# Performance work log

Hardware: AMD Instinct MI355X
Metric: run time of the kernel (lower is better)

The kernel has to match this reference:

```python
import jax, jax.numpy as jnp
import numpy as np

B, C, H, W = 16, 64, 128, 128
K = 3   # kernel_size
R = 4   # region_number
DN = ("NCHW", "OIHW", "NCHW")
PAD = [(1, 1), (1, 1)]


def leaky(x):
    return jax.nn.leaky_relu(x, 0.1)


@jax.custom_vjp
def asign_index(kernel, guide):
    # kernel: (B, R, C, H, W), guide: (B, R, H, W)
    mask = jax.nn.one_hot(jnp.argmax(guide, axis=1), guide.shape[1], axis=1, dtype=kernel.dtype)
    return jnp.sum(kernel * mask[:, :, None], axis=1)


def _asign_fwd(kernel, guide):
    return asign_index(kernel, guide), (kernel, guide)


def _asign_bwd(res, g):
    kernel, guide = res
    mask = jax.nn.one_hot(jnp.argmax(guide, axis=1), guide.shape[1], axis=1, dtype=kernel.dtype)
    grad_kernel = g[:, None] * mask[:, :, None]
    grad_guide = jnp.sum(g[:, None] * kernel, axis=2)          # (B,R,H,W)
    sm = jax.nn.softmax(guide, axis=1)                          # straight-through softmax grad
    grad_guide = sm * (grad_guide - jnp.sum(sm * grad_guide, axis=1, keepdims=True))
    return grad_kernel, grad_guide


asign_index.defvjp(_asign_fwd, _asign_bwd)


def setup_inputs() -> dict:
    key = jax.random.key(0)
    ks = jax.random.split(key, 12)
    s = 0.05
    return {
        "x0": jax.random.normal(ks[0], (B, C, H, W), jnp.float32),
        "x_deg": jax.random.normal(ks[1], (B, C), jnp.float32),
        "kw1": jax.random.normal(ks[2], (R * R, C), jnp.float32) * s,
        "kw2": jax.random.normal(ks[3], (R, C * K * K, R), jnp.float32) * s,
        "conv_w": jax.random.normal(ks[4], (C, C), jnp.float32) * s,
        "conv_b": jax.random.normal(ks[5], (C,), jnp.float32) * s,
        "ca_w1": jax.random.normal(ks[6], (R * R, C), jnp.float32) * s,
        "ca_w2": jax.random.normal(ks[7], (R, C, R), jnp.float32) * s,
        "g1_w": jax.random.normal(ks[8], (R, C, K, K), jnp.float32) * s,
        "g1_b": jax.random.normal(ks[9], (R,), jnp.float32) * s,
        "g2_w": jax.random.normal(ks[10], (R, C, K, K), jnp.float32) * s,
        "g2_b": jax.random.normal(ks[11], (R,), jnp.float32) * s,
    }


def reference(x0, x_deg, kw1, kw2, conv_w, conv_b, ca_w1, ca_w2, g1_w, g1_b, g2_w, g2_b):
    b, c, h, w = x0.shape
    # --- hypernetwork: degradation vector -> per-sample depthwise kernels ---
    h1 = leaky(x_deg @ kw1.T)                                   # (B, R*R)
    kern = jnp.einsum("bgi,goi->bgo", h1.reshape(b, R, R), kw2)  # grouped 1x1 conv1d: (B,R,C*K*K)
    kern = kern.reshape(b, R, c, K, K)
    kern = jnp.transpose(kern, (0, 2, 1, 3, 4)).reshape(b * c * R, 1, K, K)
    # per-sample-per-channel conv, R outputs per channel (groups = b*c)
    out = jax.lax.conv_general_dilated(
        x0.reshape(1, b * c, h, w), kern, (1, 1), PAD,
        dimension_numbers=DN, feature_group_count=b * c)        # (1, b*c*R, H, W)
    out = leaky(out).reshape(b, c, R, h, w).transpose(0, 2, 1, 3, 4)  # (B,R,C,H,W)
    # region routing via argmax of guide features
    guide1 = jax.lax.conv_general_dilated(x0, g1_w, (1, 1), PAD,
                                          dimension_numbers=DN) + g1_b[None, :, None, None]
    out = asign_index(out, guide1)                              # (B,C,H,W)
    # 1x1 conv (common.default_conv)
    out = jnp.einsum("bchw,oc->bohw", out, conv_w) + conv_b[None, :, None, None]
    # --- CA branch ---
    a1 = leaky(x_deg @ ca_w1.T)                                 # (B, R*R)
    att = jax.nn.sigmoid(jnp.einsum("bgi,goi->bgo", a1.reshape(b, R, R), ca_w2))  # (B,R,C)
    out2 = x0[:, None] * att[:, :, :, None, None]               # (B,R,C,H,W)
    guide2 = jax.lax.conv_general_dilated(x0, g2_w, (1, 1), PAD,
                                          dimension_numbers=DN) + g2_b[None, :, None, None]
    out2 = asign_index(out2, guide2)                            # (B,C,H,W)
    return out + out2
```

## Files before the change

kernel.cpp:

```cpp
#include <hip/hip_runtime.h>
#include <math.h>

#define Bx 16
#define Cx 64
#define Hx 128
#define Wx 128
#define HWx (Hx * Wx)

#define TW 32
#define TH 8
#define CCH 8
#define HALO_W (TW + 2)
#define HALO_H (TH + 2)
#define CPLANE (HALO_H * HALO_W)
#define CHUNK_ELEMS (CCH * CPLANE)
#define NCHUNK (Cx / CCH)

#define WS_CWB   0
#define WS_GPACK 2048
#define WS_KERN  8192
#define WS_ATT   45056

typedef short bf16x8 __attribute__((ext_vector_type(8)));
typedef float f32x4  __attribute__((ext_vector_type(4)));
typedef unsigned int u32x4 __attribute__((ext_vector_type(4)));

__device__ __host__ inline unsigned rne_bf16(float f) {
    union { float f; unsigned u; } v; v.f = f;
    return (v.u + 0x7fffu + ((v.u >> 16) & 1u)) >> 16;
}

__global__ __launch_bounds__(256)
void da_prep(const float* __restrict__ x_deg,
             const float* __restrict__ kw1,
             const float* __restrict__ kw2,
             const float* __restrict__ convw,
             const float* __restrict__ ca_w1,
             const float* __restrict__ ca_w2,
             const float* __restrict__ g1w,
             const float* __restrict__ g2w,
             float* __restrict__ ws)
{
    const int b = blockIdx.x;
    const int tid = threadIdx.x;
    unsigned int* wsu = (unsigned int*)ws;

    if (b == Bx) {
        for (int i = tid; i < 2048; i += 256) {
            const int t    = i >> 8;
            const int rem  = i & 255;
            const int lane = rem >> 2;
            const int w    = rem & 3;
            const int nt = t >> 1, ks = t & 1;
            const int o = nt * 16 + (lane & 15);
            const int c = ks * 32 + ((lane >> 4) << 3) + w * 2;
            const unsigned lo = rne_bf16(convw[o * 64 + c]);
            const unsigned hi = rne_bf16(convw[o * 64 + c + 1]);
            wsu[WS_CWB + i] = lo | (hi << 16);
        }
        for (int i = tid; i < 6144; i += 256) {
            const int c = i / 96;
            int rem = i - c * 96;
            const int rg = rem / 12;
            const int k  = rem - rg * 12;
            const int r = rg >> 1;
            const int g = rg & 1;
            const float* src = g ? g2w : g1w;
            ws[WS_GPACK + i] = (k < 9) ? src[(r * Cx + c) * 9 + k] : 0.f;
        }
        return;
    }

    __shared__ float h1[16];
    __shared__ float a1[16];
    if (tid < 32) {
        const int j = tid & 15;
        const float* wsrc = (tid < 16) ? (kw1 + j * Cx) : (ca_w1 + j * Cx);
        float acc = 0.f;
        #pragma unroll 8
        for (int c = 0; c < Cx; ++c) acc = fmaf(x_deg[b * Cx + c], wsrc[c], acc);
        acc = acc > 0.f ? acc : 0.1f * acc;
        if (tid < 16) h1[j] = acc; else a1[j] = acc;
    }
    __syncthreads();

    for (int o4 = tid; o4 < 4 * 576; o4 += 256) {
        const int g = o4 / 576;
        const int o = o4 - g * 576;
        float acc = 0.f;
        #pragma unroll
        for (int i = 0; i < 4; ++i)
            acc = fmaf(h1[g * 4 + i], kw2[(g * 576 + o) * 4 + i], acc);
        const int c = o / 9;
        const int k = o - c * 9;
        ws[WS_KERN + b * 2304 + c * 36 + k * 4 + g] = acc;
    }
    {
        const int r = tid >> 6;
        const int c = tid & 63;
        float acc = 0.f;
        #pragma unroll
        for (int i = 0; i < 4; ++i)
            acc = fmaf(a1[r * 4 + i], ca_w2[(r * Cx + c) * 4 + i], acc);
        ws[WS_ATT + b * 256 + c * 4 + r] = 1.f / (1.f + expf(-acc));
    }
}

__global__ __launch_bounds__(256, 2)
void da_main(const float* __restrict__ x0,
             const float* __restrict__ ws,
             const float* __restrict__ g1b,
             const float* __restrict__ g2b,
             const float* __restrict__ convb,
             float* __restrict__ out)
{
    const int b  = blockIdx.z;
    const int h0 = blockIdx.y * TH;
    const int w0 = blockIdx.x * TW;
    const int tid = threadIdx.x;
    const int tx = tid & (TW - 1);
    const int ty = tid >> 5;
    const int lane = tid & 63;
    const int wave = tid >> 6;

    __shared__ __align__(16) float swts[6656];
    __shared__ __align__(16) float sxy[4352];
    __shared__ __align__(16) unsigned int rbuf_u[8192];

    const float* xb  = x0 + (size_t)b * Cx * HWx;
    const float* kws = ws + WS_KERN + b * 2304;
    const float* aws = ws + WS_ATT  + b * 256;
    const unsigned int* wsu = (const unsigned int*)ws;

    int o0, o1, o2, o3, o4, o5, o6, o7, o8, o9, o10;
    unsigned vmask = 0u;
#define MKOFF(i, oname)                                                        \
    do {                                                                       \
        const int e   = tid + (i) * 256;                                       \
        const int cc  = e / CPLANE;                                            \
        const int rem = e - cc * CPLANE;                                       \
        const int row = rem / HALO_W;                                          \
        const int col = rem - row * HALO_W;                                    \
        const int gh  = h0 - 1 + row;                                          \
        const int gw  = w0 - 1 + col;                                          \
        oname = cc * HWx + gh * Wx + gw;                                       \
        if (e < CHUNK_ELEMS && (unsigned)gh < Hx && (unsigned)gw < Wx)         \
            vmask |= (1u << (i));                                              \
    } while (0)
    MKOFF(0, o0);  MKOFF(1, o1);  MKOFF(2, o2);  MKOFF(3, o3);
    MKOFF(4, o4);  MKOFF(5, o5);  MKOFF(6, o6);  MKOFF(7, o7);
    MKOFF(8, o8);  MKOFF(9, o9);  MKOFF(10, o10);
#undef MKOFF

#define STAGE_CHUNK(ch)                                                        \
    do {                                                                       \
        const float* src = xb + (size_t)(ch) * CCH * HWx;                      \
        float v0 = 0.f, v1 = 0.f, v2 = 0.f, v3 = 0.f, v4 = 0.f, v5 = 0.f;     \
        float v6 = 0.f, v7 = 0.f, v8 = 0.f, v9 = 0.f, v10 = 0.f;              \
        if (vmask & 1u)      v0  = src[o0];                                    \
        if (vmask & 2u)      v1  = src[o1];                                    \
        if (vmask & 4u)      v2  = src[o2];                                    \
        if (vmask & 8u)      v3  = src[o3];                                    \
        if (vmask & 16u)     v4  = src[o4];                                    \
        if (vmask & 32u)     v5  = src[o5];                                    \
        if (vmask & 64u)     v6  = src[o6];                                    \
        if (vmask & 128u)    v7  = src[o7];                                    \
        if (vmask & 256u)    v8  = src[o8];                                    \
        if (vmask & 512u)    v9  = src[o9];                                    \
        if (vmask & 1024u)   v10 = src[o10];                                   \
        sxy[tid]          = v0;   sxy[tid + 256]  = v1;                        \
        sxy[tid + 512]    = v2;   sxy[tid + 768]  = v3;                        \
        sxy[tid + 1024]   = v4;   sxy[tid + 1280] = v5;                        \
        sxy[tid + 1536]   = v6;   sxy[tid + 1792] = v7;                        \
        sxy[tid + 2048]   = v8;   sxy[tid + 2304] = v9;                        \
        if (tid < CHUNK_ELEMS - 2560) sxy[tid + 2560] = v10;                   \
    } while (0)

    {
        const float4* s4 = (const float4*)(ws + WS_GPACK);
        float4* d4 = (float4*)swts;
        const float4 g0 = s4[tid], g1 = s4[tid + 256], g2 = s4[tid + 512];
        const float4 g3 = s4[tid + 768], g4 = s4[tid + 1024], g5 = s4[tid + 1280];
        d4[tid] = g0; d4[tid + 256] = g1; d4[tid + 512] = g2;
        d4[tid + 768] = g3; d4[tid + 1024] = g4; d4[tid + 1280] = g5;
    }

    float ga[8];
    #pragma unroll
    for (int r = 0; r < 4; ++r) { ga[r] = g1b[r]; ga[4 + r] = g2b[r]; }

    #pragma unroll 1
    for (int ch = 0; ch < NCHUNK; ++ch) {
        __syncthreads();
        STAGE_CHUNK(ch);
        __syncthreads();

        float pg[8] = {0.f, 0.f, 0.f, 0.f, 0.f, 0.f, 0.f, 0.f};
        #pragma unroll
        for (int cc = 0; cc < CCH; ++cc) {
            const int c = ch * CCH + cc;
            float n[9];
            #pragma unroll
            for (int kh = 0; kh < 3; ++kh)
                #pragma unroll
                for (int kw = 0; kw < 3; ++kw)
                    n[kh * 3 + kw] = sxy[cc * CPLANE + (ty + kh) * HALO_W + (tx + kw)];
            const float4* gpv = (const float4*)(swts + c * 96);
            #pragma unroll
            for (int rg = 0; rg < 8; ++rg) {
                const float4 q0 = gpv[rg * 3 + 0];
                const float4 q1 = gpv[rg * 3 + 1];
                const float4 q2 = gpv[rg * 3 + 2];
                float s = 0.f;
                s = fmaf(n[0], q0.x, s); s = fmaf(n[1], q0.y, s); s = fmaf(n[2], q0.z, s);
                s = fmaf(n[3], q0.w, s); s = fmaf(n[4], q1.x, s); s = fmaf(n[5], q1.y, s);
                s = fmaf(n[6], q1.z, s); s = fmaf(n[7], q1.w, s); s = fmaf(n[8], q2.x, s);
                pg[(rg >> 1) + (rg & 1) * 4] += s;
            }
        }
        #pragma unroll
        for (int i = 0; i < 8; ++i) ga[i] += pg[i];
    }

    int r1 = 0, r2 = 0;
    {
        float m = ga[0];
        #pragma unroll
        for (int r = 1; r < 4; ++r) if (ga[r] > m) { m = ga[r]; r1 = r; }
        float m2 = ga[4];
        #pragma unroll
        for (int r = 1; r < 4; ++r) if (ga[4 + r] > m2) { m2 = ga[4 + r]; r2 = r; }
    }

    __syncthreads();
    {
        const float4* k4 = (const float4*)kws;
        const float4 k0 = k4[tid], k1 = k4[tid + 256];
        const float kt = kws[2048 + tid];
        const float at = aws[tid];
        float4* kd4 = (float4*)swts;
        kd4[tid] = k0; kd4[tid + 256] = k1;
        swts[2048 + tid] = kt;
        swts[2304 + tid] = at;
    }

    #pragma unroll 1
    for (int ch = 0; ch < NCHUNK; ++ch) {
        __syncthreads();
        STAGE_CHUNK(ch);
        __syncthreads();

        unsigned int us[4] = {0u, 0u, 0u, 0u};
        #pragma unroll
        for (int cc = 0; cc < CCH; ++cc) {
            const int c = ch * CCH + cc;
            float n[9];
            #pragma unroll
            for (int kh = 0; kh < 3; ++kh)
                #pragma unroll
                for (int kw = 0; kw < 3; ++kw)
                    n[kh * 3 + kw] = sxy[cc * CPLANE + (ty + kh) * HALO_W + (tx + kw)];

            float dw = 0.f;
            #pragma unroll
            for (int k = 0; k < 9; ++k)
                dw = fmaf(n[k], swts[c * 36 + k * 4 + r1], dw);
            const float routed = dw > 0.f ? dw : 0.1f * dw;

            us[cc >> 1] |= rne_bf16(routed) << ((cc & 1) * 16);
        }
        {
            const int byteoff = wave * 8192 + lane * 128 + ((ch * 16) ^ ((lane & 7) << 4));
            *(u32x4*)((char*)rbuf_u + byteoff) = (u32x4){us[0], us[1], us[2], us[3]};
        }
    }
    __syncthreads();

    float y[Cx];
    {
        f32x4 acc[4][4];
        #pragma unroll
        for (int mt = 0; mt < 4; ++mt)
            #pragma unroll
            for (int nt = 0; nt < 4; ++nt)
                acc[mt][nt] = (f32x4){0.f, 0.f, 0.f, 0.f};

        const bf16x8* bglob = (const bf16x8*)(wsu + WS_CWB);
        #pragma unroll
        for (int ks = 0; ks < 2; ++ks) {
            bf16x8 av[4];
            #pragma unroll
            for (int mt = 0; mt < 4; ++mt) {
                const int pix = mt * 16 + (lane & 15);
                const int byteoff = wave * 8192 + pix * 128 +
                    ((ks * 64 + ((lane >> 4) * 16)) ^ ((pix & 7) << 4));
                av[mt] = *(const bf16x8*)((const char*)rbuf_u + byteoff);
            }
            bf16x8 bv[4];
            #pragma unroll
            for (int nt = 0; nt < 4; ++nt)
                bv[nt] = bglob[(nt * 2 + ks) * 64 + lane];
            #pragma unroll
            for (int mt = 0; mt < 4; ++mt)
                #pragma unroll
                for (int nt = 0; nt < 4; ++nt)
                    acc[mt][nt] = __builtin_amdgcn_mfma_f32_16x16x32_bf16(
                        av[mt], bv[nt], acc[mt][nt], 0, 0, 0);
        }

        #pragma unroll
        for (int nt = 0; nt < 4; ++nt) {
            #pragma unroll
            for (int mt = 0; mt < 4; ++mt)
                #pragma unroll
                for (int q = 0; q < 4; ++q)
                    sxy[wave * 1088 + (mt * 16 + (lane >> 4) * 4 + q) * 17 + (lane & 15)]
                        = acc[mt][nt][q];
            #pragma unroll
            for (int t = 0; t < 16; ++t)
                y[nt * 16 + t] = sxy[wave * 1088 + lane * 17 + t];
        }
    }

    const int hh = h0 + ty;
    const int ww = w0 + tx;
    float* op = out + (size_t)b * Cx * HWx + hh * Wx + ww;
    const float* xp = xb + hh * Wx + ww;
    #pragma unroll
    for (int o = 0; o < Cx; ++o) {
        const float v = y[o] + convb[o] + xp[(size_t)o * HWx] * swts[2304 + o * 4 + r2];
        op[(size_t)o * HWx] = v;
    }
}

extern "C" void kernel_launch(void* const* d_in, const int* in_sizes, int n_in,
                              void* d_out, int out_size, void* d_ws, size_t ws_size,
                              hipStream_t stream) {
    const float* x0     = (const float*)d_in[0];
    const float* x_deg  = (const float*)d_in[1];
    const float* kw1    = (const float*)d_in[2];
    const float* kw2    = (const float*)d_in[3];
    const float* convw  = (const float*)d_in[4];
    const float* convb  = (const float*)d_in[5];
    const float* ca_w1  = (const float*)d_in[6];
    const float* ca_w2  = (const float*)d_in[7];
    const float* g1w    = (const float*)d_in[8];
    const float* g1b    = (const float*)d_in[9];
    const float* g2w    = (const float*)d_in[10];
    const float* g2b    = (const float*)d_in[11];
    float* outp = (float*)d_out;
    float* wsf  = (float*)d_ws;

    da_prep<<<Bx + 1, 256, 0, stream>>>(x_deg, kw1, kw2, convw, ca_w1, ca_w2,
                                        g1w, g2w, wsf);

    dim3 grid(Wx / TW, Hx / TH, Bx);
    da_main<<<grid, 256, 0, stream>>>(x0, wsf, g1b, g2b, convb, outp);
}
```

Before: 146.0 us.

## Shrink LDS footprint by splitting guide weights and reusing rbuf for transpose

Repacks the guide conv weights into a k-major layout without padding (72 floats per channel) and stages them into shared memory in two halves, the second half loaded mid-loop at chunk 4. The epilogue transpose scratch now reuses each wave's own rbuf region, and the __syncthreads before the MFMA stage is removed because each wave only reads its own region. LDS drops from about 77KB to about 53KB, meant to allow more resident blocks per CU, and the inner guide loop is restructured so all eight accumulators take the same neighbor value. The risks are a race from loading the second weight half while other waves might still read the first, and a missing barrier if any cross-wave dependency remains.

```diff
diff --git a/kernel.cpp b/kernel.cpp
--- a/kernel.cpp
+++ b/kernel.cpp
@@ -18,8 +18,8 @@
 
 #define WS_CWB   0
 #define WS_GPACK 2048
-#define WS_KERN  8192
-#define WS_ATT   45056
+#define WS_KERN  6656
+#define WS_ATT   43520
 
 typedef short bf16x8 __attribute__((ext_vector_type(8)));
 typedef float f32x4  __attribute__((ext_vector_type(4)));
@@ -58,15 +58,15 @@
             const unsigned hi = rne_bf16(convw[o * 64 + c + 1]);
             wsu[WS_CWB + i] = lo | (hi << 16);
         }
-        for (int i = tid; i < 6144; i += 256) {
-            const int c = i / 96;
-            int rem = i - c * 96;
-            const int rg = rem / 12;
-            const int k  = rem - rg * 12;
+        for (int i = tid; i < 4608; i += 256) {
+            const int c = i / 72;
+            const int rem = i - c * 72;
+            const int k  = rem >> 3;
+            const int rg = rem & 7;
             const int r = rg >> 1;
             const int g = rg & 1;
             const float* src = g ? g2w : g1w;
-            ws[WS_GPACK + i] = (k < 9) ? src[(r * Cx + c) * 9 + k] : 0.f;
+            ws[WS_GPACK + i] = src[(r * Cx + c) * 9 + k];
         }
         return;
     }
@@ -123,9 +123,10 @@
     const int lane = tid & 63;
     const int wave = tid >> 6;
 
-    __shared__ __align__(16) float swts[6656];
-    __shared__ __align__(16) float sxy[4352];
-    __shared__ __align__(16) unsigned int rbuf_u[8192];
+    __shared__ __align__(16) float swts[2560];
+    __shared__ __align__(16) char pool[10880 + 32768];
+    float* sx = (float*)pool;
+    char*  rbuf = pool + 10880;
 
     const float* xb  = x0 + (size_t)b * Cx * HWx;
     const float* kws = ws + WS_KERN + b * 2304;
@@ -168,22 +169,27 @@
         if (vmask & 256u)    v8  = src[o8];                                    \
         if (vmask & 512u)    v9  = src[o9];                                    \
         if (vmask & 1024u)   v10 = src[o10];                                   \
-        sxy[tid]          = v0;   sxy[tid + 256]  = v1;                        \
-        sxy[tid + 512]    = v2;   sxy[tid + 768]  = v3;                        \
-        sxy[tid + 1024]   = v4;   sxy[tid + 1280] = v5;                        \
-        sxy[tid + 1536]   = v6;   sxy[tid + 1792] = v7;                        \
-        sxy[tid + 2048]   = v8;   sxy[tid + 2304] = v9;                        \
-        if (tid < CHUNK_ELEMS - 2560) sxy[tid + 2560] = v10;                   \
+        sx[tid]           = v0;   sx[tid + 256]  = v1;                         \
+        sx[tid + 512]     = v2;   sx[tid + 768]  = v3;                         \
+        sx[tid + 1024]    = v4;   sx[tid + 1280] = v5;                         \
+        sx[tid + 1536]    = v6;   sx[tid + 1792] = v7;                         \
+        sx[tid + 2048]    = v8;   sx[tid + 2304] = v9;                         \
+        if (tid < CHUNK_ELEMS - 2560) sx[tid + 2560] = v10;                    \
     } while (0)
 
-    {
-        const float4* s4 = (const float4*)(ws + WS_GPACK);
-        float4* d4 = (float4*)swts;
-        const float4 g0 = s4[tid], g1 = s4[tid + 256], g2 = s4[tid + 512];
-        const float4 g3 = s4[tid + 768], g4 = s4[tid + 1024], g5 = s4[tid + 1280];
-        d4[tid] = g0; d4[tid + 256] = g1; d4[tid + 512] = g2;
-        d4[tid + 768] = g3; d4[tid + 1024] = g4; d4[tid + 1280] = g5;
-    }
+#define STAGE_GPACK(halfbase)                                                  \
+    do {                                                                       \
+        const float4* s4 = (const float4*)(ws + WS_GPACK + (halfbase));       \
+        float4* d4 = (float4*)swts;                                            \
+        const float4 g0 = s4[tid];                                             \
+        const float4 g1 = s4[tid + 256];                                       \
+        float4 g2;                                                             \
+        if (tid < 64) g2 = s4[tid + 512];                                      \
+        d4[tid] = g0; d4[tid + 256] = g1;                                      \
+        if (tid < 64) d4[tid + 512] = g2;                                      \
+    } while (0)
+
+    STAGE_GPACK(0);
 
     float ga[8];
     #pragma unroll
@@ -193,6 +199,7 @@
     for (int ch = 0; ch < NCHUNK; ++ch) {
         __syncthreads();
         STAGE_CHUNK(ch);
+        if (ch == 4) STAGE_GPACK(2304);
         __syncthreads();
 
         float pg[8] = {0.f, 0.f, 0.f, 0.f, 0.f, 0.f, 0.f, 0.f};
@@ -204,19 +211,26 @@
             for (int kh = 0; kh < 3; ++kh)
                 #pragma unroll
                 for (int kw = 0; kw < 3; ++kw)
-                    n[kh * 3 + kw] = sxy[cc * CPLANE + (ty + kh) * HALO_W + (tx + kw)];
-            const float4* gpv = (const float4*)(swts + c * 96);
-            #pragma unroll
-            for (int rg = 0; rg < 8; ++rg) {
-                const float4 q0 = gpv[rg * 3 + 0];
-                const float4 q1 = gpv[rg * 3 + 1];
-                const float4 q2 = gpv[rg * 3 + 2];
-                float s = 0.f;
-                s = fmaf(n[0], q0.x, s); s = fmaf(n[1], q0.y, s); s = fmaf(n[2], q0.z, s);
-                s = fmaf(n[3], q0.w, s); s = fmaf(n[4], q1.x, s); s = fmaf(n[5], q1.y, s);
-                s = fmaf(n[6], q1.z, s); s = fmaf(n[7], q1.w, s); s = fmaf(n[8], q2.x, s);
-                pg[(rg >> 1) + (rg & 1) * 4] += s;
+                    n[kh * 3 + kw] = sx[cc * CPLANE + (ty + kh) * HALO_W + (tx + kw)];
+            const float4* wp = (const float4*)(swts + (c & 31) * 72);
+            float a8[8] = {0.f, 0.f, 0.f, 0.f, 0.f, 0.f, 0.f, 0.f};
+            #pragma unroll
+            for (int k = 0; k < 9; ++k) {
+                const float4 wa = wp[k * 2];
+                const float4 wb = wp[k * 2 + 1];
+                a8[0] = fmaf(n[k], wa.x, a8[0]);
+                a8[1] = fmaf(n[k], wa.y, a8[1]);
+                a8[2] = fmaf(n[k], wa.z, a8[2]);
+                a8[3] = fmaf(n[k], wa.w, a8[3]);
+                a8[4] = fmaf(n[k], wb.x, a8[4]);
+                a8[5] = fmaf(n[k], wb.y, a8[5]);
+                a8[6] = fmaf(n[k], wb.z, a8[6]);
+                a8[7] = fmaf(n[k], wb.w, a8[7]);
             }
+            pg[0] += a8[0]; pg[4] += a8[1];
+            pg[1] += a8[2]; pg[5] += a8[3];
+            pg[2] += a8[4]; pg[6] += a8[5];
+            pg[3] += a8[6]; pg[7] += a8[7];
         }
         #pragma unroll
         for (int i = 0; i < 8; ++i) ga[i] += pg[i];
@@ -259,7 +273,7 @@
             for (int kh = 0; kh < 3; ++kh)
                 #pragma unroll
                 for (int kw = 0; kw < 3; ++kw)
-                    n[kh * 3 + kw] = sxy[cc * CPLANE + (ty + kh) * HALO_W + (tx + kw)];
+                    n[kh * 3 + kw] = sx[cc * CPLANE + (ty + kh) * HALO_W + (tx + kw)];
 
             float dw = 0.f;
             #pragma unroll
@@ -271,10 +285,9 @@
         }
         {
             const int byteoff = wave * 8192 + lane * 128 + ((ch * 16) ^ ((lane & 7) << 4));
-            *(u32x4*)((char*)rbuf_u + byteoff) = (u32x4){us[0], us[1], us[2], us[3]};
-        }
-    }
-    __syncthreads();
+            *(u32x4*)(rbuf + byteoff) = (u32x4){us[0], us[1], us[2], us[3]};
+        }
+    }
 
     float y[Cx];
     {
@@ -294,7 +307,7 @@
                 const int pix = mt * 16 + (lane & 15);
                 const int byteoff = wave * 8192 + pix * 128 +
                     ((ks * 64 + ((lane >> 4) * 16)) ^ ((pix & 7) << 4));
-                av[mt] = *(const bf16x8*)((const char*)rbuf_u + byteoff);
+                av[mt] = *(const bf16x8*)(rbuf + byteoff);
             }
             bf16x8 bv[4];
             #pragma unroll
@@ -308,17 +321,17 @@
                         av[mt], bv[nt], acc[mt][nt], 0, 0, 0);
         }
 
+        float* syw = (float*)(rbuf + wave * 8192);
         #pragma unroll
         for (int nt = 0; nt < 4; ++nt) {
             #pragma unroll
             for (int mt = 0; mt < 4; ++mt)
                 #pragma unroll
                 for (int q = 0; q < 4; ++q)
-                    sxy[wave * 1088 + (mt * 16 + (lane >> 4) * 4 + q) * 17 + (lane & 15)]
-                        = acc[mt][nt][q];
+                    syw[(mt * 16 + (lane >> 4) * 4 + q) * 17 + (lane & 15)] = acc[mt][nt][q];
             #pragma unroll
             for (int t = 0; t < 16; ++t)
-                y[nt * 16 + t] = sxy[wave * 1088 + lane * 17 + t];
+                y[nt * 16 + t] = syw[lane * 17 + t];
         }
     }
 
```

Result: slower. 171.3 us (+17.3%).
